# Kernel optimization log

Measured on AMD Instinct MI355X. Metric: run time of the kernel, lower is better.

The kernel has to match this reference:

```python
import jax, jax.numpy as jnp
import numpy as np
from jax import lax

RANK = 2
INPUT_SIZE = 8
HIDDEN_SIZE = 1024
NUM_MIXTURES = 4
ALPHA = 0.1
BASE_SCALE = 500.0
D = 2 * RANK + INPUT_SIZE  # 12
BATCH, SEQ_LEN = 64, 512


def setup_inputs() -> dict:
    key = jax.random.key(0)
    k1, k2, k3, k4, k5 = jax.random.split(key, 5)
    return {
        "x": jax.random.normal(k1, (BATCH, SEQ_LEN, INPUT_SIZE), jnp.float32),
        "eps": jax.random.normal(k2, (NUM_MIXTURES, HIDDEN_SIZE, D), jnp.float32),
        "means": jax.random.normal(k3, (NUM_MIXTURES, D), jnp.float32),
        "scale_tril_raw": jax.random.normal(k4, (NUM_MIXTURES, D, D), jnp.float32) / np.sqrt(HIDDEN_SIZE),
        "mixture_weights": jax.random.uniform(k5, (NUM_MIXTURES,), jnp.float32),
    }


def reference(x, eps, means, scale_tril_raw, mixture_weights):
    # _clamp_tril: lower-triangular with strictly positive diagonal
    diag = jnp.abs(jnp.diagonal(scale_tril_raw, axis1=-2, axis2=-1) - 1e-12) + 1e-12  # [K,D]
    L = jnp.tril(scale_tril_raw, -1) + diag[..., None] * jnp.eye(D, dtype=scale_tril_raw.dtype)
    # _normalize_weights
    w = jnp.clip(mixture_weights, 1e-6, None)
    w = w / jnp.sum(w)
    # rsample: mean + eps @ L^T, per mixture -> [K, H, D]
    samp = means[:, None, :] + jnp.einsum('khd,ked->khe', eps, L)
    mixed = jnp.einsum('k,khd->hd', w, samp)  # weighted sum over mixtures [H, D]
    m = mixed[:, :RANK]            # [H, r]
    n = mixed[:, RANK:2 * RANK]    # [H, r]
    I = mixed[:, 2 * RANK:]        # [H, input_size]
    J = (m @ n.T) * (BASE_SCALE / HIDDEN_SIZE)  # [H, H]
    span = jnp.concatenate([m, I], axis=1)      # [H, r + input_size]

    def step(h, x_t):
        dh = -h + jnp.tanh(h) @ J.T + x_t @ I.T
        h_new = h + ALPHA * dh
        return h_new, h_new

    h0 = jnp.zeros((x.shape[0], HIDDEN_SIZE), x.dtype)
    _, hs = lax.scan(step, h0, jnp.swapaxes(x, 0, 1))  # hs: [T, B, H]
    hiddens = jnp.swapaxes(hs, 0, 1)                   # [B, T, H]
    pinv = jnp.linalg.pinv(span)                       # [r+input_size, H]
    return jnp.einsum('dh,bth->btd', pinv, hiddens)    # [B, T, r+input_size]
```

## Files before the change

kernel.cpp:

```cpp
#include <hip/hip_runtime.h>

#define HS   1024
#define SEQ  512
#define NBAT 64
#define INSZ 8
#define NM   4
#define DD   12

#define DPP_ADD(v, ctrl, rmask, bmask) \
  v += __int_as_float(__builtin_amdgcn_update_dpp(0, __float_as_int(v), ctrl, rmask, bmask, true))

__device__ __forceinline__ void wave64_sum2(float &a, float &b){
  DPP_ADD(a, 0x111, 0xf, 0xf); DPP_ADD(b, 0x111, 0xf, 0xf);
  DPP_ADD(a, 0x112, 0xf, 0xf); DPP_ADD(b, 0x112, 0xf, 0xf);
  DPP_ADD(a, 0x114, 0xf, 0xe); DPP_ADD(b, 0x114, 0xf, 0xe);
  DPP_ADD(a, 0x118, 0xf, 0xc); DPP_ADD(b, 0x118, 0xf, 0xc);
  DPP_ADD(a, 0x142, 0xa, 0xf); DPP_ADD(b, 0x142, 0xa, 0xf);
  DPP_ADD(a, 0x143, 0xc, 0xf); DPP_ADD(b, 0x143, 0xc, 0xf);
}

__device__ __forceinline__ float fast_tanh(float x){
  float e = __expf(x + x);
  float r = __builtin_amdgcn_rcpf(e + 1.0f);
  return __builtin_fmaf(-2.0f, r, 1.0f);
}

__global__ __launch_bounds__(256,1)
void rnn_scan(const float* __restrict__ x,
              const float* __restrict__ eps,
              const float* __restrict__ means,
              const float* __restrict__ tril,
              const float* __restrict__ mw,
              float* __restrict__ out)
{
  const int b    = blockIdx.x;
  const int tid  = threadIdx.x;
  const int wave = tid >> 6;
  const int lane = tid & 63;

  __shared__ float  xs[SEQ*INSZ];
  __shared__ float2 red[2][4];
  __shared__ __align__(16) float outb[SEQ*10];

  float w[NM];
  {
    float s = 0.f;
    #pragma unroll
    for (int k=0;k<NM;k++){ w[k] = fmaxf(mw[k], 1e-6f); s += w[k]; }
    float inv = 1.0f/s;
    #pragma unroll
    for (int k=0;k<NM;k++) w[k] *= inv;
  }

  float m0[4],m1[4],n0[4],n1[4],h[4];
  float2 Im2[4][4];
  #pragma unroll
  for (int j=0;j<4;j++){
    const int i = tid + j*256;
    float ep[NM][DD];
    #pragma unroll
    for (int k=0;k<NM;k++)
      #pragma unroll
      for (int d=0;d<DD;d++)
        ep[k][d] = eps[(k*HS + i)*DD + d];
    float mix[DD];
    #pragma unroll
    for (int e=0;e<DD;e++){
      float a = 0.f;
      #pragma unroll
      for (int k=0;k<NM;k++){
        float se = means[k*DD+e];
        for (int d=0; d<e; d++)
          se += ep[k][d]*tril[(k*DD+e)*DD + d];
        float dg = fabsf(tril[(k*DD+e)*DD + e] - 1e-12f) + 1e-12f;
        se += ep[k][e]*dg;
        a += w[k]*se;
      }
      mix[e] = a;
    }
    m0[j]=mix[0]; m1[j]=mix[1]; n0[j]=mix[2]; n1[j]=mix[3];
    #pragma unroll
    for (int e=0;e<4;e++) Im2[j][e]=make_float2(mix[4+2*e], mix[5+2*e]);
    h[j]=0.f;
  }

  for (int idx=tid; idx<SEQ*INSZ; idx+=256) xs[idx] = x[b*SEQ*INSZ + idx];
  __syncthreads();

  const float alpha = 0.1f;
  const float oma   = 0.9f;
  const float scl   = 500.0f/1024.0f;
  const float as    = alpha*scl;
  float o = 0.f;
  const float2* xs2 = (const float2*)xs;

  #pragma unroll 2
  for (int t=0;t<SEQ;t++){
    float u0=0.f, u1=0.f;
    #pragma unroll
    for (int j=0;j<4;j++){
      float th = fast_tanh(h[j]);
      u0 = __builtin_fmaf(th, n0[j], u0);
      u1 = __builtin_fmaf(th, n1[j], u1);
    }
    wave64_sum2(u0, u1);
    if (lane==63) red[t&1][wave] = make_float2(u0,u1);

    float inj[4];
    #pragma unroll
    for (int j=0;j<4;j++){
      float2 acc = make_float2(0.f,0.f);
      #pragma unroll
      for (int e=0;e<4;e++){
        float2 xe = xs2[t*4+e];
        acc.x = __builtin_fmaf(xe.x, Im2[j][e].x, acc.x);
        acc.y = __builtin_fmaf(xe.y, Im2[j][e].y, acc.y);
      }
      inj[j] = acc.x + acc.y;
    }

    __syncthreads();
    float2 r0=red[t&1][0], r1=red[t&1][1], r2=red[t&1][2], r3=red[t&1][3];
    float U0 = (r0.x+r1.x)+(r2.x+r3.x);
    float U1 = (r0.y+r1.y)+(r2.y+r3.y);

    #pragma unroll
    for (int j=0;j<4;j++){
      float mu = __builtin_fmaf(m1[j], U1, m0[j]*U0);
      h[j] = __builtin_fmaf(oma, h[j],
             __builtin_fmaf(as, mu, alpha*inj[j]));
    }

    if (tid < 10){
      float add = (tid==0) ? scl*U0 : (tid==1) ? scl*U1 : xs[t*8 + tid-2];
      o = __builtin_fmaf(oma, o, alpha*add);
      outb[t*10+tid] = o;
    }
  }

  __syncthreads();
  const float4* ob4 = (const float4*)outb;
  float4* o4 = (float4*)out + b*(SEQ*10/4);
  for (int idx=tid; idx<SEQ*10/4; idx+=256) o4[idx] = ob4[idx];
}

extern "C" void kernel_launch(void* const* d_in, const int* in_sizes, int n_in,
                              void* d_out, int out_size, void* d_ws, size_t ws_size,
                              hipStream_t stream) {
  const float* x     = (const float*)d_in[0];
  const float* eps   = (const float*)d_in[1];
  const float* means = (const float*)d_in[2];
  const float* tril  = (const float*)d_in[3];
  const float* mw    = (const float*)d_in[4];
  float* out = (float*)d_out;

  rnn_scan<<<NBAT, 256, 0, stream>>>(x, eps, means, tril, mw, out);
}
```

Baseline: 289.2 us.

## Reformulate RNN scan in low-rank state with single-wave blocks and precomputed input drive

Rewrites the recurrence so the hidden state is tracked through two low-rank scalars (A, B) plus a filtered input Y. The tanh argument is then rebuilt as m0*A + m1*B + I*Y per unit, and the reduction is handled by one 64-lane wave with readlane, which removes the block-wide __syncthreads on every step. When the workspace is large enough, a separate kernel first writes the input-driven term C[b,t,:] to global memory and the scan streams it with prefetch. This trades a large extra memory write and read for less per-step arithmetic. Tanh is computed through exp2 and rcp, with scale factors folded into the constants.

Result: slower. 381.0 us (+31.8%).

```diff
diff --git a/kernel.cpp b/kernel.cpp
--- a/kernel.cpp
+++ b/kernel.cpp
@@ -6,6 +6,26 @@
 #define INSZ 8
 #define NM   4
 #define DD   12
+
+#define ALPHA 0.1f
+#define OMA   0.9f
+#define SCL   (500.0f/1024.0f)
+#define AS    (ALPHA*SCL)
+
+#if __has_builtin(__builtin_amdgcn_exp2f)
+  #define GS 2.8853900817779268f
+  #define EXPG(v) __builtin_amdgcn_exp2f(v)
+#else
+  #define GS 2.0f
+  #define EXPG(v) __expf(v)
+#endif
+
+typedef float f2 __attribute__((ext_vector_type(2)));
+__device__ __forceinline__ f2 mk2(float a, float b){ f2 r; r.x=a; r.y=b; return r; }
+__device__ __forceinline__ f2 splat2(float a){ return mk2(a,a); }
+__device__ __forceinline__ f2 fma2(f2 a, f2 b, f2 c){
+  f2 r; r.x=fmaf(a.x,b.x,c.x); r.y=fmaf(a.y,b.y,c.y); return r;
+}
 
 #define DPP_ADD(v, ctrl, rmask, bmask) \
   v += __int_as_float(__builtin_amdgcn_update_dpp(0, __float_as_int(v), ctrl, rmask, bmask, true))
@@ -18,130 +38,214 @@
   DPP_ADD(a, 0x142, 0xa, 0xf); DPP_ADD(b, 0x142, 0xa, 0xf);
   DPP_ADD(a, 0x143, 0xc, 0xf); DPP_ADD(b, 0x143, 0xc, 0xf);
 }
-
-__device__ __forceinline__ float fast_tanh(float x){
-  float e = __expf(x + x);
-  float r = __builtin_amdgcn_rcpf(e + 1.0f);
-  return __builtin_fmaf(-2.0f, r, 1.0f);
+#define RD63(v) __int_as_float(__builtin_amdgcn_readlane(__float_as_int(v), 63))
+
+template<int E0, int E1>
+__device__ __forceinline__ void mix_unit(int i, const float* __restrict__ eps,
+                                         const float* __restrict__ means,
+                                         const float* __restrict__ tril,
+                                         const float* w, float* outm){
+  float ep[NM][DD];
+  #pragma unroll
+  for (int k=0;k<NM;k++){
+    const float4* p = (const float4*)(eps + (size_t)(k*HS + i)*DD);
+    float4 r0=p[0], r1=p[1], r2=p[2];
+    ep[k][0]=r0.x; ep[k][1]=r0.y; ep[k][2]=r0.z; ep[k][3]=r0.w;
+    ep[k][4]=r1.x; ep[k][5]=r1.y; ep[k][6]=r1.z; ep[k][7]=r1.w;
+    ep[k][8]=r2.x; ep[k][9]=r2.y; ep[k][10]=r2.z; ep[k][11]=r2.w;
+  }
+  #pragma unroll
+  for (int e=E0;e<E1;e++){
+    float a = 0.f;
+    #pragma unroll
+    for (int k=0;k<NM;k++){
+      float se = means[k*DD+e];
+      #pragma unroll
+      for (int d=0; d<e; d++) se = fmaf(ep[k][d], tril[(k*DD+e)*DD+d], se);
+      float dg = fabsf(tril[(k*DD+e)*DD+e] - 1e-12f) + 1e-12f;
+      se = fmaf(ep[k][e], dg, se);
+      a = fmaf(w[k], se, a);
+    }
+    outm[e-E0] = a;
+  }
 }
 
 __global__ __launch_bounds__(256,1)
-void rnn_scan(const float* __restrict__ x,
-              const float* __restrict__ eps,
-              const float* __restrict__ means,
-              const float* __restrict__ tril,
-              const float* __restrict__ mw,
-              float* __restrict__ out)
+void gemm_c(const float* __restrict__ x, const float* __restrict__ eps,
+            const float* __restrict__ means, const float* __restrict__ tril,
+            const float* __restrict__ mw, float* __restrict__ C)
 {
-  const int b    = blockIdx.x;
-  const int tid  = threadIdx.x;
-  const int wave = tid >> 6;
-  const int lane = tid & 63;
-
-  __shared__ float  xs[SEQ*INSZ];
-  __shared__ float2 red[2][4];
+  const int b = blockIdx.x >> 2, q = blockIdx.x & 3;
+  const int tid = threadIdx.x;
+  __shared__ float xs[SEQ*INSZ];
+  __shared__ float yb[128][8];
+
+  float w[NM];
+  { float s=0.f;
+    #pragma unroll
+    for (int k=0;k<NM;k++){ w[k]=fmaxf(mw[k],1e-6f); s+=w[k]; }
+    float inv=1.0f/s;
+    #pragma unroll
+    for (int k=0;k<NM;k++) w[k]*=inv; }
+
+  float I[4][8];
+  #pragma unroll
+  for (int j=0;j<4;j++) mix_unit<4,12>(tid*4+j, eps, means, tril, w, I[j]);
+
+  { const float4* xp=(const float4*)(x + (size_t)b*SEQ*INSZ);
+    float4* xd=(float4*)xs;
+    for (int idx=tid; idx<SEQ*INSZ/4; idx+=256) xd[idx]=xp[idx]; }
+  __syncthreads();
+
+  if (tid < 8){
+    float Y=0.f; const int t0=q*128, tend=t0+128;
+    for (int t=0;t<tend;t++){
+      if (t>=t0) yb[t-t0][tid]=Y;
+      Y = fmaf(OMA, Y, (GS*ALPHA)*xs[t*8+tid]);
+    }
+  }
+  __syncthreads();
+
+  float* Cb = C + ((size_t)b*SEQ + (size_t)q*128)*HS + tid*4;
+  for (int tt=0; tt<128; tt++){
+    float4 ya=((float4*)yb[tt])[0], yc=((float4*)yb[tt])[1];
+    float cv[4];
+    #pragma unroll
+    for (int j=0;j<4;j++){
+      float a =       I[j][0]*ya.x;
+      a = fmaf(I[j][1],ya.y,a); a = fmaf(I[j][2],ya.z,a); a = fmaf(I[j][3],ya.w,a);
+      a = fmaf(I[j][4],yc.x,a); a = fmaf(I[j][5],yc.y,a);
+      a = fmaf(I[j][6],yc.z,a); a = fmaf(I[j][7],yc.w,a);
+      cv[j]=a;
+    }
+    *(float4*)(Cb + (size_t)tt*HS) = make_float4(cv[0],cv[1],cv[2],cv[3]);
+  }
+}
+
+template<int PRE>
+__global__ __launch_bounds__(64,1)
+void rnn_scan(const float* __restrict__ x, const float* __restrict__ eps,
+              const float* __restrict__ means, const float* __restrict__ tril,
+              const float* __restrict__ mw, float* __restrict__ out,
+              const float* __restrict__ C)
+{
+  const int b = blockIdx.x;
+  const int lane = threadIdx.x;
+
+  __shared__ float xs[SEQ*INSZ];
   __shared__ __align__(16) float outb[SEQ*10];
 
   float w[NM];
-  {
-    float s = 0.f;
-    #pragma unroll
-    for (int k=0;k<NM;k++){ w[k] = fmaxf(mw[k], 1e-6f); s += w[k]; }
-    float inv = 1.0f/s;
-    #pragma unroll
-    for (int k=0;k<NM;k++) w[k] *= inv;
-  }
-
-  float m0[4],m1[4],n0[4],n1[4],h[4];
-  float2 Im2[4][4];
-  #pragma unroll
-  for (int j=0;j<4;j++){
-    const int i = tid + j*256;
-    float ep[NM][DD];
-    #pragma unroll
-    for (int k=0;k<NM;k++)
+  { float s=0.f;
+    #pragma unroll
+    for (int k=0;k<NM;k++){ w[k]=fmaxf(mw[k],1e-6f); s+=w[k]; }
+    float inv=1.0f/s;
+    #pragma unroll
+    for (int k=0;k<NM;k++) w[k]*=inv; }
+
+  f2 m0v[8], m1v[8], n0v[8], n1v[8];
+  float sn0=0.f, sn1=0.f;
+  #pragma unroll
+  for (int p=0;p<8;p++){
+    float mA[4], mB[4];
+    mix_unit<0,4>(16*lane+2*p,   eps, means, tril, w, mA);
+    mix_unit<0,4>(16*lane+2*p+1, eps, means, tril, w, mB);
+    m0v[p]=mk2(mA[0],mB[0]); m1v[p]=mk2(mA[1],mB[1]);
+    sn0 += mA[2]+mB[2];      sn1 += mA[3]+mB[3];
+    n0v[p]=mk2(-2.f*mA[2], -2.f*mB[2]);
+    n1v[p]=mk2(-2.f*mA[3], -2.f*mB[3]);
+  }
+  wave64_sum2(sn0, sn1);
+  const float N0 = RD63(sn0), N1 = RD63(sn1);
+
+  f2 Iv[8][8]; float Yg[8];
+  const float AG = GS*ALPHA;
+  if constexpr(!PRE){
+    #pragma unroll
+    for (int p=0;p<8;p++){
+      float IA[8], IB[8];
+      mix_unit<4,12>(16*lane+2*p,   eps, means, tril, w, IA);
+      mix_unit<4,12>(16*lane+2*p+1, eps, means, tril, w, IB);
       #pragma unroll
-      for (int d=0;d<DD;d++)
-        ep[k][d] = eps[(k*HS + i)*DD + d];
-    float mix[DD];
-    #pragma unroll
-    for (int e=0;e<DD;e++){
-      float a = 0.f;
-      #pragma unroll
-      for (int k=0;k<NM;k++){
-        float se = means[k*DD+e];
-        for (int d=0; d<e; d++)
-          se += ep[k][d]*tril[(k*DD+e)*DD + d];
-        float dg = fabsf(tril[(k*DD+e)*DD + e] - 1e-12f) + 1e-12f;
-        se += ep[k][e]*dg;
-        a += w[k]*se;
-      }
-      mix[e] = a;
-    }
-    m0[j]=mix[0]; m1[j]=mix[1]; n0[j]=mix[2]; n1[j]=mix[3];
-    #pragma unroll
-    for (int e=0;e<4;e++) Im2[j][e]=make_float2(mix[4+2*e], mix[5+2*e]);
-    h[j]=0.f;
-  }
-
-  for (int idx=tid; idx<SEQ*INSZ; idx+=256) xs[idx] = x[b*SEQ*INSZ + idx];
-  __syncthreads();
-
-  const float alpha = 0.1f;
-  const float oma   = 0.9f;
-  const float scl   = 500.0f/1024.0f;
-  const float as    = alpha*scl;
-  float o = 0.f;
-  const float2* xs2 = (const float2*)xs;
-
-  #pragma unroll 2
-  for (int t=0;t<SEQ;t++){
-    float u0=0.f, u1=0.f;
-    #pragma unroll
-    for (int j=0;j<4;j++){
-      float th = fast_tanh(h[j]);
-      u0 = __builtin_fmaf(th, n0[j], u0);
-      u1 = __builtin_fmaf(th, n1[j], u1);
-    }
-    wave64_sum2(u0, u1);
-    if (lane==63) red[t&1][wave] = make_float2(u0,u1);
-
-    float inj[4];
-    #pragma unroll
-    for (int j=0;j<4;j++){
-      float2 acc = make_float2(0.f,0.f);
-      #pragma unroll
-      for (int e=0;e<4;e++){
-        float2 xe = xs2[t*4+e];
-        acc.x = __builtin_fmaf(xe.x, Im2[j][e].x, acc.x);
-        acc.y = __builtin_fmaf(xe.y, Im2[j][e].y, acc.y);
-      }
-      inj[j] = acc.x + acc.y;
-    }
-
-    __syncthreads();
-    float2 r0=red[t&1][0], r1=red[t&1][1], r2=red[t&1][2], r3=red[t&1][3];
-    float U0 = (r0.x+r1.x)+(r2.x+r3.x);
-    float U1 = (r0.y+r1.y)+(r2.y+r3.y);
-
-    #pragma unroll
-    for (int j=0;j<4;j++){
-      float mu = __builtin_fmaf(m1[j], U1, m0[j]*U0);
-      h[j] = __builtin_fmaf(oma, h[j],
-             __builtin_fmaf(as, mu, alpha*inj[j]));
-    }
-
-    if (tid < 10){
-      float add = (tid==0) ? scl*U0 : (tid==1) ? scl*U1 : xs[t*8 + tid-2];
-      o = __builtin_fmaf(oma, o, alpha*add);
-      outb[t*10+tid] = o;
-    }
-  }
+      for (int e=0;e<8;e++) Iv[p][e]=mk2(IA[e],IB[e]);
+    }
+    #pragma unroll
+    for (int e=0;e<8;e++) Yg[e]=0.f;
+  }
+
+  { const float4* xp=(const float4*)(x + (size_t)b*SEQ*INSZ);
+    float4* xd=(float4*)xs;
+    for (int idx=lane; idx<SEQ*INSZ/4; idx+=64) xd[idx]=xp[idx]; }
+  __syncthreads();
+
+  const float CA = GS*AS;
+  float A=0.f, Bst=0.f, o=0.f;
+
+  const float4* Cp = PRE ? ((const float4*)C + (size_t)b*SEQ*(HS/4) + lane*4)
+                         : (const float4*)nullptr;
+  #define CLOAD(v0,v1,v2,v3,T) { const float4* p_ = Cp + (size_t)(T)*(HS/4); \
+    v0=p_[0]; v1=p_[1]; v2=p_[2]; v3=p_[3]; }
+
+  float4 c00{},c01{},c02{},c03{}, c10{},c11{},c12{},c13{},
+         c20{},c21{},c22{},c23{}, c30{},c31{},c32{},c33{};
+  if constexpr(PRE){
+    CLOAD(c00,c01,c02,c03,0) CLOAD(c10,c11,c12,c13,1)
+    CLOAD(c20,c21,c22,c23,2) CLOAD(c30,c31,c32,c33,3)
+  }
+
+  #define STEP(T, TN, v0,v1,v2,v3) { \
+    f2 g[8]; \
+    if constexpr(PRE){ \
+      g[0]=mk2(v0.x,v0.y); g[1]=mk2(v0.z,v0.w); \
+      g[2]=mk2(v1.x,v1.y); g[3]=mk2(v1.z,v1.w); \
+      g[4]=mk2(v2.x,v2.y); g[5]=mk2(v2.z,v2.w); \
+      g[6]=mk2(v3.x,v3.y); g[7]=mk2(v3.z,v3.w); \
+    } else { \
+      _Pragma("unroll") for (int p=0;p<8;p++){ \
+        f2 a = mk2(0.f,0.f); \
+        _Pragma("unroll") for (int e=0;e<8;e++) a = fma2(Iv[p][e], splat2(Yg[e]), a); \
+        g[p]=a; } \
+    } \
+    { f2 A2=splat2(A), B2=splat2(Bst); \
+      _Pragma("unroll") for (int p=0;p<8;p++){ \
+        g[p]=fma2(m0v[p],A2,g[p]); g[p]=fma2(m1v[p],B2,g[p]); } } \
+    if constexpr(PRE){ CLOAD(v0,v1,v2,v3,TN) } \
+    else { float4 xa=((const float4*)xs)[(T)*2], xb=((const float4*)xs)[(T)*2+1]; \
+      Yg[0]=fmaf(OMA,Yg[0],AG*xa.x); Yg[1]=fmaf(OMA,Yg[1],AG*xa.y); \
+      Yg[2]=fmaf(OMA,Yg[2],AG*xa.z); Yg[3]=fmaf(OMA,Yg[3],AG*xa.w); \
+      Yg[4]=fmaf(OMA,Yg[4],AG*xb.x); Yg[5]=fmaf(OMA,Yg[5],AG*xb.y); \
+      Yg[6]=fmaf(OMA,Yg[6],AG*xb.z); Yg[7]=fmaf(OMA,Yg[7],AG*xb.w); } \
+    f2 ua=mk2(0.f,0.f), ub=mk2(0.f,0.f); \
+    _Pragma("unroll") for (int p=0;p<8;p++){ \
+      f2 ex = mk2(EXPG(g[p].x), EXPG(g[p].y)); \
+      f2 dd = mk2(ex.x+1.f, ex.y+1.f); \
+      f2 rr = mk2(__builtin_amdgcn_rcpf(dd.x), __builtin_amdgcn_rcpf(dd.y)); \
+      ua = fma2(rr, n0v[p], ua); ub = fma2(rr, n1v[p], ub); } \
+    float u0=ua.x+ua.y, u1=ub.x+ub.y; \
+    wave64_sum2(u0,u1); \
+    float U0 = N0 + RD63(u0); \
+    float U1 = N1 + RD63(u1); \
+    A   = fmaf(CA,U0, 0.9f*A); \
+    Bst = fmaf(CA,U1, 0.9f*Bst); \
+    if (lane<10){ \
+      float add = lane==0 ? SCL*U0 : lane==1 ? SCL*U1 : xs[(T)*8+lane-2]; \
+      o = fmaf(OMA, o, ALPHA*add); outb[(T)*10+lane]=o; } \
+  }
+
+  #pragma unroll 1
+  for (int t=0; t<SEQ; t+=4){
+    STEP(t,   (t+4)&(SEQ-1), c00,c01,c02,c03)
+    STEP(t+1, (t+5)&(SEQ-1), c10,c11,c12,c13)
+    STEP(t+2, (t+6)&(SEQ-1), c20,c21,c22,c23)
+    STEP(t+3, (t+7)&(SEQ-1), c30,c31,c32,c33)
+  }
+  #undef STEP
+  #undef CLOAD
 
   __syncthreads();
   const float4* ob4 = (const float4*)outb;
-  float4* o4 = (float4*)out + b*(SEQ*10/4);
-  for (int idx=tid; idx<SEQ*10/4; idx+=256) o4[idx] = ob4[idx];
+  float4* o4 = (float4*)out + (size_t)b*(SEQ*10/4);
+  for (int idx=lane; idx<SEQ*10/4; idx+=64) o4[idx]=ob4[idx];
 }
 
 extern "C" void kernel_launch(void* const* d_in, const int* in_sizes, int n_in,
@@ -154,5 +258,11 @@
   const float* mw    = (const float*)d_in[4];
   float* out = (float*)d_out;
 
-  rnn_scan<<<NBAT, 256, 0, stream>>>(x, eps, means, tril, mw, out);
-}
+  const size_t cbytes = (size_t)NBAT*SEQ*HS*sizeof(float);
+  if (d_ws && ws_size >= cbytes){
+    gemm_c<<<NBAT*4, 256, 0, stream>>>(x, eps, means, tril, mw, (float*)d_ws);
+    rnn_scan<1><<<NBAT, 64, 0, stream>>>(x, eps, means, tril, mw, out, (const float*)d_ws);
+  } else {
+    rnn_scan<0><<<NBAT, 64, 0, stream>>>(x, eps, means, tril, mw, out, nullptr);
+  }
+}
```
